# Performance work log

Hardware: AMD Instinct MI355X
Metric: run time of the kernel (lower is better)

The kernel has to match this reference:

```python
import jax, jax.numpy as jnp
import numpy as np
from jax import lax

B, C_IN, HC, H, W, K = 32, 32, 64, 64, 64, 3


def _conv(x, w, b):
    # x: [B,C,H,W], w: [O,I,K,K] -> [B,O,H,W] (stride 1, pad 1)
    y = lax.conv_general_dilated(x, w, window_strides=(1, 1), padding=[(1, 1), (1, 1)],
                                 dimension_numbers=("NCHW", "OIHW", "NCHW"))
    return y + b[None, :, None, None]


def setup_inputs() -> dict:
    key = jax.random.key(0)
    ks = jax.random.split(key, 20)
    d = {
        "x": jax.random.normal(ks[0], (B, C_IN, H, W), jnp.float32),
        "hidden_state": jax.random.normal(ks[1], (B, HC, H, W), jnp.float32),
        "cell_state": jax.random.normal(ks[2], (B, HC, H, W), jnp.float32),
    }
    sx = 1.0 / np.sqrt(C_IN * K * K)
    sh = 1.0 / np.sqrt(HC * K * K)
    names_x = ["w_xi", "w_xf", "w_xo", "w_xg"]
    names_h = ["w_hi", "w_hf", "w_ho", "w_hg"]
    for i, n in enumerate(names_x):
        d[n] = jax.random.uniform(ks[3 + i], (HC, C_IN, K, K), jnp.float32, -sx, sx)
        d["b" + n[1:]] = jax.random.uniform(ks[7 + i], (HC,), jnp.float32, -sx, sx)
    for i, n in enumerate(names_h):
        d[n] = jax.random.uniform(ks[11 + i], (HC, HC, K, K), jnp.float32, -sh, sh)
        d["b" + n[1:]] = jax.random.uniform(ks[15 + i], (HC,), jnp.float32, -sh, sh)
    return d


def reference(x, hidden_state, cell_state,
              w_xi, w_xf, w_xo, w_xg, b_xi, b_xf, b_xo, b_xg,
              w_hi, w_hf, w_ho, w_hg, b_hi, b_hf, b_ho, b_hg):
    Wx = jnp.concatenate([w_xi, w_xf, w_xo, w_xg], axis=0)
    bx = jnp.concatenate([b_xi, b_xf, b_xo, b_xg], axis=0)
    Wh = jnp.concatenate([w_hi, w_hf, w_ho, w_hg], axis=0)
    bh = jnp.concatenate([b_hi, b_hf, b_ho, b_hg], axis=0)
    gates = _conv(x, Wx, bx) + _conv(hidden_state, Wh, bh)  # [B,4*HC,H,W]
    zi, zf, zo, zg = jnp.split(gates, 4, axis=1)
    i = jax.nn.sigmoid(zi)
    f = jax.nn.sigmoid(zf)
    o = jax.nn.sigmoid(zo)
    g = jnp.tanh(zg)
    c_new = f * cell_state + i * g
    h_new = o * jnp.tanh(c_new)
    return (h_new, c_new)
```

## Files before the change

### kernel.cpp

```cpp
#include <hip/hip_runtime.h>


#define B_   32
#define CIN  32
#define HC_  64
#define HH   64
#define WW   64

#define A_ELEMS (9 * 6 * 8 * 64 * 8)
#define P_ROW   (12 * 66 * 8)
#define AKK     4096
#define BLDS    25344

typedef __attribute__((ext_vector_type(8)))  short  short8;
typedef __attribute__((ext_vector_type(16))) float  floatx16;

struct PackArgs {
    const float* wx[4]; const float* wh[4];
    const float* bx[4]; const float* bh[4];
};

__device__ __forceinline__ short f2bf(float f) {
    unsigned u = __float_as_uint(f);
    u += 0x7FFFu + ((u >> 16) & 1u);
    return (short)(u >> 16);
}

__device__ __forceinline__ void gl_lds16(const short* g, short* l) {
    __builtin_amdgcn_global_load_lds(
        (const __attribute__((address_space(1))) unsigned int*)g,
        (__attribute__((address_space(3))) unsigned int*)l, 16, 0, 0);
}

__global__ __launch_bounds__(256) void pack_weights(PackArgs pa, short* a_pk, float* bias) {
    int idx = blockIdx.x * 256 + threadIdx.x;
    if (idx < A_ELEMS) {
        int j    = idx & 7;
        int lane = (idx >> 3) & 63;
        int rest = idx >> 9;
        int s    = rest & 7;
        int rest2 = rest >> 3;
        int kk   = rest2 % 6;
        int tap  = rest2 / 6;
        int og = s >> 1, fi = s & 1;
        int m32 = lane & 31;
        int gate = 2 * fi + (m32 >> 4);
        int oc   = og * 16 + (m32 & 15);
        int c    = kk * 16 + (lane >> 5) * 8 + j;
        int ky = tap / 3, kx = tap - 3 * ky;
        float v = (c < CIN)
            ? pa.wx[gate][((oc * CIN + c) * 3 + ky) * 3 + kx]
            : pa.wh[gate][((oc * HC_ + (c - CIN)) * 3 + ky) * 3 + kx];
        a_pk[idx] = f2bf(v);
    }
    if (idx < 256) {
        int gate = idx >> 6, oc = idx & 63;
        bias[idx] = pa.bx[gate][oc] + pa.bh[gate][oc];
    }
}

__global__ __launch_bounds__(256) void pack_input(const float* __restrict__ x,
                                                  const float* __restrict__ h,
                                                  short* __restrict__ P) {
    const int yy = blockIdx.x, b = blockIdx.y;
    int4* prow4 = (int4*)(P + ((size_t)b * 66 + yy) * P_ROW);

    if (yy == 0 || yy == 65) {
        int4 z = {0, 0, 0, 0};
        for (int g = threadIdx.x; g < 792; g += 256) prow4[g] = z;
        return;
    }

    __shared__ short t[64 * 98];
    const int y = yy - 1;
    const int col = threadIdx.x & 63, cg = threadIdx.x >> 6;
    for (int c = cg; c < 96; c += 4) {
        float v = (c < CIN) ? x[((b * CIN + c) * HH + y) * WW + col]
                            : h[((b * HC_ + (c - CIN)) * HH + y) * WW + col];
        t[col * 98 + c] = f2bf(v);
    }
    __syncthreads();

    for (int g = threadIdx.x; g < 792; g += 256) {
        int pc = g / 66, xx = g - 66 * pc;
        int4 val = {0, 0, 0, 0};
        if (xx >= 1 && xx <= 64) {
            const short* sp = &t[(xx - 1) * 98 + pc * 8];
            val.x = *(const int*)(sp + 0); val.y = *(const int*)(sp + 2);
            val.z = *(const int*)(sp + 4); val.w = *(const int*)(sp + 6);
        }
        prow4[g] = val;
    }
}

__global__ __launch_bounds__(512, 4) void convlstm_main(
    const short* __restrict__ P, const short* __restrict__ a_pk,
    const float* __restrict__ bias, const float* __restrict__ cell,
    float* __restrict__ out)
{
    __shared__ __align__(16) short lds[BLDS + 3 * AKK];

    const int tid = threadIdx.x;
    const int b  = blockIdx.x >> 5;
    const int y0 = (blockIdx.x & 31) * 2;

    const int wv = tid >> 6, lane = tid & 63;
    const int ln31 = lane & 31, hg = lane >> 5;
    const int og = wv & 3, nh = wv >> 2;
    const int y = y0 + nh;

    floatx16 acc[2][2];
    #pragma unroll
    for (int fi = 0; fi < 2; ++fi)
        #pragma unroll
        for (int ns = 0; ns < 2; ++ns)
            #pragma unroll
            for (int q = 0; q < 16; ++q) acc[fi][ns][q] = 0.f;

    short* Asl = lds + BLDS;
    const int a_rd  = og * 1024 + lane * 8;
    const int b_rd  = nh * 6336 + hg * 528 + ln31 * 8;

    {
        const short* Bsrc = P + ((size_t)(b * 66) + y0) * P_ROW;
        #pragma unroll
        for (int i = 0; i < 7; ++i) {
            int id = i * 512 + tid;
            if (id < 3168)
                gl_lds16(Bsrc + id * 8, lds + (i * 512 + wv * 64) * 8);
        }
        gl_lds16(a_pk + tid * 8,       Asl + wv * 64 * 8);
        gl_lds16(a_pk + AKK + tid * 8, Asl + AKK + wv * 64 * 8);
    }
    asm volatile("s_waitcnt vmcnt(1)" ::: "memory");
    __builtin_amdgcn_s_barrier();
    __builtin_amdgcn_sched_barrier(0);

    #pragma unroll
    for (int c = 0; c < 54; ++c) {
        const int tap = c / 6, kk = c % 6;
        const int ky = tap / 3, kx = tap % 3;

        if (c < 52)
            gl_lds16(a_pk + (c + 2) * AKK + tid * 8,
                     Asl + ((c + 2) % 3) * AKK + wv * 64 * 8);

        const short* Ab = Asl + (c % 3) * AKK;
        const short* Bb = lds + b_rd + ky * 6336 + kk * 1056 + kx * 8;

        short8 a0 = *(const short8*)&Ab[a_rd];
        short8 a1 = *(const short8*)&Ab[a_rd + 512];
        short8 b0 = *(const short8*)&Bb[0];
        short8 b1 = *(const short8*)&Bb[256];
        acc[0][0] = __builtin_amdgcn_mfma_f32_32x32x16_bf16(a0, b0, acc[0][0], 0, 0, 0);
        acc[0][1] = __builtin_amdgcn_mfma_f32_32x32x16_bf16(a0, b1, acc[0][1], 0, 0, 0);
        acc[1][0] = __builtin_amdgcn_mfma_f32_32x32x16_bf16(a1, b0, acc[1][0], 0, 0, 0);
        acc[1][1] = __builtin_amdgcn_mfma_f32_32x32x16_bf16(a1, b1, acc[1][1], 0, 0, 0);

        if (c < 52)       asm volatile("s_waitcnt vmcnt(1)" ::: "memory");
        else if (c == 52) asm volatile("s_waitcnt vmcnt(0)" ::: "memory");
        if (c < 53) {
            __builtin_amdgcn_s_barrier();
            __builtin_amdgcn_sched_barrier(0);
        }
    }

    const size_t plane = (size_t)B_ * HC_ * HH * WW;
    #pragma unroll
    for (int q = 0; q < 4; ++q)
    #pragma unroll
    for (int b8 = 0; b8 < 2; ++b8) {
        const int oc16 = q + 4 * hg + 8 * b8;
        const int oc = og * 16 + oc16;
        const float Bi = bias[oc],       Bf = bias[64 + oc];
        const float Bo = bias[128 + oc], Bg = bias[192 + oc];
        const int r_lo = q + 4 * b8, r_hi = q + 4 * (2 + b8);
        #pragma unroll
        for (int ns = 0; ns < 2; ++ns) {
            float zi = acc[0][ns][r_lo] + Bi;
            float zf = acc[0][ns][r_hi] + Bf;
            float zo = acc[1][ns][r_lo] + Bo;
            float zg = acc[1][ns][r_hi] + Bg;
            float ig = 1.f / (1.f + __expf(-zi));
            float fg = 1.f / (1.f + __expf(-zf));
            float sg = 1.f / (1.f + __expf(-zo));
            float e2 = __expf(2.f * zg);
            float gg = 1.f - 2.f / (e2 + 1.f);
            const int x = ns * 32 + ln31;
            size_t off = ((size_t)(b * HC_ + oc) * HH + y) * WW + x;
            float cn = fg * cell[off] + ig * gg;
            float ec = __expf(2.f * cn);
            out[off] = sg * (1.f - 2.f / (ec + 1.f));
            out[plane + off] = cn;
        }
    }
}

extern "C" void kernel_launch(void* const* d_in, const int* in_sizes, int n_in,
                              void* d_out, int out_size, void* d_ws, size_t ws_size,
                              hipStream_t stream) {
    PackArgs pa;
    pa.wx[0] = (const float*)d_in[3];  pa.bx[0] = (const float*)d_in[4];
    pa.wx[1] = (const float*)d_in[5];  pa.bx[1] = (const float*)d_in[6];
    pa.wx[2] = (const float*)d_in[7];  pa.bx[2] = (const float*)d_in[8];
    pa.wx[3] = (const float*)d_in[9];  pa.bx[3] = (const float*)d_in[10];
    pa.wh[0] = (const float*)d_in[11]; pa.bh[0] = (const float*)d_in[12];
    pa.wh[1] = (const float*)d_in[13]; pa.bh[1] = (const float*)d_in[14];
    pa.wh[2] = (const float*)d_in[15]; pa.bh[2] = (const float*)d_in[16];
    pa.wh[3] = (const float*)d_in[17]; pa.bh[3] = (const float*)d_in[18];

    short* a_pk = (short*)d_ws;
    float* bias = (float*)((char*)d_ws + A_ELEMS * sizeof(short));
    short* P    = (short*)((char*)d_ws + 443392);

    pack_weights<<<dim3(A_ELEMS / 256), dim3(256), 0, stream>>>(pa, a_pk, bias);
    pack_input <<<dim3(66, B_), dim3(256), 0, stream>>>(
        (const float*)d_in[0], (const float*)d_in[1], P);
    convlstm_main<<<dim3(B_ * 32), dim3(512), 0, stream>>>(
        P, a_pk, bias, (const float*)d_in[2], (float*)d_out);
}
```

Baseline: 222.6 us.

## Shrink main kernel to four waves each computing two output rows

New measurement: 223.4 us. About the same (+0.4%).

```diff
diff --git a/kernel.cpp b/kernel.cpp
--- a/kernel.cpp
+++ b/kernel.cpp
@@ -93,7 +93,7 @@
     }
 }
 
-__global__ __launch_bounds__(512, 4) void convlstm_main(
+__global__ __launch_bounds__(256, 2) void convlstm_main(
     const short* __restrict__ P, const short* __restrict__ a_pk,
     const float* __restrict__ bias, const float* __restrict__ cell,
     float* __restrict__ out)
@@ -106,33 +106,38 @@
 
     const int wv = tid >> 6, lane = tid & 63;
     const int ln31 = lane & 31, hg = lane >> 5;
-    const int og = wv & 3, nh = wv >> 2;
-    const int y = y0 + nh;
-
-    floatx16 acc[2][2];
+    const int og = wv;
+
+    floatx16 acc[2][2][2];
     #pragma unroll
     for (int fi = 0; fi < 2; ++fi)
         #pragma unroll
-        for (int ns = 0; ns < 2; ++ns)
+        for (int rr = 0; rr < 2; ++rr)
             #pragma unroll
-            for (int q = 0; q < 16; ++q) acc[fi][ns][q] = 0.f;
+            for (int ns = 0; ns < 2; ++ns)
+                #pragma unroll
+                for (int q = 0; q < 16; ++q) acc[fi][rr][ns][q] = 0.f;
 
     short* Asl = lds + BLDS;
-    const int a_rd  = og * 1024 + lane * 8;
-    const int b_rd  = nh * 6336 + hg * 528 + ln31 * 8;
+    const int a_rd   = og * 1024 + lane * 8;
+    const int b_lane = hg * 528 + ln31 * 8;
 
     {
         const short* Bsrc = P + ((size_t)(b * 66) + y0) * P_ROW;
         #pragma unroll
-        for (int i = 0; i < 7; ++i) {
-            int id = i * 512 + tid;
+        for (int i = 0; i < 13; ++i) {
+            int id = i * 256 + tid;
             if (id < 3168)
-                gl_lds16(Bsrc + id * 8, lds + (i * 512 + wv * 64) * 8);
-        }
-        gl_lds16(a_pk + tid * 8,       Asl + wv * 64 * 8);
-        gl_lds16(a_pk + AKK + tid * 8, Asl + AKK + wv * 64 * 8);
-    }
-    asm volatile("s_waitcnt vmcnt(1)" ::: "memory");
+                gl_lds16(Bsrc + id * 8, lds + (i * 256 + wv * 64) * 8);
+        }
+        #pragma unroll
+        for (int ck = 0; ck < 2; ++ck)
+            #pragma unroll
+            for (int i = 0; i < 2; ++i)
+                gl_lds16(a_pk + ck * AKK + (i * 256 + tid) * 8,
+                         Asl + ck * AKK + (i * 256 + wv * 64) * 8);
+    }
+    asm volatile("s_waitcnt vmcnt(2)" ::: "memory");
     __builtin_amdgcn_s_barrier();
     __builtin_amdgcn_sched_barrier(0);
 
@@ -141,23 +146,35 @@
         const int tap = c / 6, kk = c % 6;
         const int ky = tap / 3, kx = tap % 3;
 
-        if (c < 52)
-            gl_lds16(a_pk + (c + 2) * AKK + tid * 8,
-                     Asl + ((c + 2) % 3) * AKK + wv * 64 * 8);
-
-        const short* Ab = Asl + (c % 3) * AKK;
-        const short* Bb = lds + b_rd + ky * 6336 + kk * 1056 + kx * 8;
-
-        short8 a0 = *(const short8*)&Ab[a_rd];
-        short8 a1 = *(const short8*)&Ab[a_rd + 512];
-        short8 b0 = *(const short8*)&Bb[0];
-        short8 b1 = *(const short8*)&Bb[256];
-        acc[0][0] = __builtin_amdgcn_mfma_f32_32x32x16_bf16(a0, b0, acc[0][0], 0, 0, 0);
-        acc[0][1] = __builtin_amdgcn_mfma_f32_32x32x16_bf16(a0, b1, acc[0][1], 0, 0, 0);
-        acc[1][0] = __builtin_amdgcn_mfma_f32_32x32x16_bf16(a1, b0, acc[1][0], 0, 0, 0);
-        acc[1][1] = __builtin_amdgcn_mfma_f32_32x32x16_bf16(a1, b1, acc[1][1], 0, 0, 0);
-
-        if (c < 52)       asm volatile("s_waitcnt vmcnt(1)" ::: "memory");
+        if (c < 52) {
+            const short* src = a_pk + (c + 2) * AKK;
+            short* dst = Asl + ((c + 2) % 3) * AKK;
+            gl_lds16(src + tid * 8,         dst + (wv * 64) * 8);
+            gl_lds16(src + (256 + tid) * 8, dst + (256 + wv * 64) * 8);
+        }
+
+        const short* Ab = Asl + (c % 3) * AKK + a_rd;
+        const short* Bb = lds + b_lane + ky * 6336 + 2 * kk * 528 + kx * 8;
+
+        short8 a0  = *(const short8*)&Ab[0];
+        short8 a1  = *(const short8*)&Ab[512];
+        short8 b00 = *(const short8*)&Bb[0];
+        short8 b01 = *(const short8*)&Bb[256];
+        short8 b10 = *(const short8*)&Bb[6336];
+        short8 b11 = *(const short8*)&Bb[6336 + 256];
+
+        __builtin_amdgcn_s_setprio(1);
+        acc[0][0][0] = __builtin_amdgcn_mfma_f32_32x32x16_bf16(a0, b00, acc[0][0][0], 0, 0, 0);
+        acc[0][0][1] = __builtin_amdgcn_mfma_f32_32x32x16_bf16(a0, b01, acc[0][0][1], 0, 0, 0);
+        acc[0][1][0] = __builtin_amdgcn_mfma_f32_32x32x16_bf16(a0, b10, acc[0][1][0], 0, 0, 0);
+        acc[0][1][1] = __builtin_amdgcn_mfma_f32_32x32x16_bf16(a0, b11, acc[0][1][1], 0, 0, 0);
+        acc[1][0][0] = __builtin_amdgcn_mfma_f32_32x32x16_bf16(a1, b00, acc[1][0][0], 0, 0, 0);
+        acc[1][0][1] = __builtin_amdgcn_mfma_f32_32x32x16_bf16(a1, b01, acc[1][0][1], 0, 0, 0);
+        acc[1][1][0] = __builtin_amdgcn_mfma_f32_32x32x16_bf16(a1, b10, acc[1][1][0], 0, 0, 0);
+        acc[1][1][1] = __builtin_amdgcn_mfma_f32_32x32x16_bf16(a1, b11, acc[1][1][1], 0, 0, 0);
+        __builtin_amdgcn_s_setprio(0);
+
+        if (c < 52)       asm volatile("s_waitcnt vmcnt(2)" ::: "memory");
         else if (c == 52) asm volatile("s_waitcnt vmcnt(0)" ::: "memory");
         if (c < 53) {
             __builtin_amdgcn_s_barrier();
@@ -176,17 +193,20 @@
         const float Bo = bias[128 + oc], Bg = bias[192 + oc];
         const int r_lo = q + 4 * b8, r_hi = q + 4 * (2 + b8);
         #pragma unroll
+        for (int rr = 0; rr < 2; ++rr)
+        #pragma unroll
         for (int ns = 0; ns < 2; ++ns) {
-            float zi = acc[0][ns][r_lo] + Bi;
-            float zf = acc[0][ns][r_hi] + Bf;
-            float zo = acc[1][ns][r_lo] + Bo;
-            float zg = acc[1][ns][r_hi] + Bg;
+            float zi = acc[0][rr][ns][r_lo] + Bi;
+            float zf = acc[0][rr][ns][r_hi] + Bf;
+            float zo = acc[1][rr][ns][r_lo] + Bo;
+            float zg = acc[1][rr][ns][r_hi] + Bg;
             float ig = 1.f / (1.f + __expf(-zi));
             float fg = 1.f / (1.f + __expf(-zf));
             float sg = 1.f / (1.f + __expf(-zo));
             float e2 = __expf(2.f * zg);
             float gg = 1.f - 2.f / (e2 + 1.f);
             const int x = ns * 32 + ln31;
+            const int y = y0 + rr;
             size_t off = ((size_t)(b * HC_ + oc) * HH + y) * WW + x;
             float cn = fg * cell[off] + ig * gg;
             float ec = __expf(2.f * cn);
@@ -216,6 +236,6 @@
     pack_weights<<<dim3(A_ELEMS / 256), dim3(256), 0, stream>>>(pa, a_pk, bias);
     pack_input <<<dim3(66, B_), dim3(256), 0, stream>>>(
         (const float*)d_in[0], (const float*)d_in[1], P);
-    convlstm_main<<<dim3(B_ * 32), dim3(512), 0, stream>>>(
+    convlstm_main<<<dim3(B_ * 32), dim3(256), 0, stream>>>(
         P, a_pk, bias, (const float*)d_in[2], (float*)d_out);
 }
```

## Read weight fragments directly from global memory instead of LDS ring buffer

Applied to the files above, without the earlier changes.

Result: slower. 245.8 us (+10.4%).

```diff
diff --git a/kernel.cpp b/kernel.cpp
--- a/kernel.cpp
+++ b/kernel.cpp
@@ -98,7 +98,7 @@
     const float* __restrict__ bias, const float* __restrict__ cell,
     float* __restrict__ out)
 {
-    __shared__ __align__(16) short lds[BLDS + 3 * AKK];
+    __shared__ __align__(16) short lds[BLDS];
 
     const int tid = threadIdx.x;
     const int b  = blockIdx.x >> 5;
@@ -117,9 +117,8 @@
             #pragma unroll
             for (int q = 0; q < 16; ++q) acc[fi][ns][q] = 0.f;
 
-    short* Asl = lds + BLDS;
-    const int a_rd  = og * 1024 + lane * 8;
-    const int b_rd  = nh * 6336 + hg * 528 + ln31 * 8;
+    const short* Ag  = a_pk + og * 1024 + lane * 8;
+    const int    b_rd = nh * 6336 + hg * 528 + ln31 * 8;
 
     {
         const short* Bsrc = P + ((size_t)(b * 66) + y0) * P_ROW;
@@ -129,39 +128,24 @@
             if (id < 3168)
                 gl_lds16(Bsrc + id * 8, lds + (i * 512 + wv * 64) * 8);
         }
-        gl_lds16(a_pk + tid * 8,       Asl + wv * 64 * 8);
-        gl_lds16(a_pk + AKK + tid * 8, Asl + AKK + wv * 64 * 8);
-    }
-    asm volatile("s_waitcnt vmcnt(1)" ::: "memory");
-    __builtin_amdgcn_s_barrier();
-    __builtin_amdgcn_sched_barrier(0);
-
-    #pragma unroll
-    for (int c = 0; c < 54; ++c) {
-        const int tap = c / 6, kk = c % 6;
+    }
+    __syncthreads();
+
+    for (int tap = 0; tap < 9; ++tap) {
         const int ky = tap / 3, kx = tap % 3;
-
-        if (c < 52)
-            gl_lds16(a_pk + (c + 2) * AKK + tid * 8,
-                     Asl + ((c + 2) % 3) * AKK + wv * 64 * 8);
-
-        const short* Ab = Asl + (c % 3) * AKK;
-        const short* Bb = lds + b_rd + ky * 6336 + kk * 1056 + kx * 8;
-
-        short8 a0 = *(const short8*)&Ab[a_rd];
-        short8 a1 = *(const short8*)&Ab[a_rd + 512];
-        short8 b0 = *(const short8*)&Bb[0];
-        short8 b1 = *(const short8*)&Bb[256];
-        acc[0][0] = __builtin_amdgcn_mfma_f32_32x32x16_bf16(a0, b0, acc[0][0], 0, 0, 0);
-        acc[0][1] = __builtin_amdgcn_mfma_f32_32x32x16_bf16(a0, b1, acc[0][1], 0, 0, 0);
-        acc[1][0] = __builtin_amdgcn_mfma_f32_32x32x16_bf16(a1, b0, acc[1][0], 0, 0, 0);
-        acc[1][1] = __builtin_amdgcn_mfma_f32_32x32x16_bf16(a1, b1, acc[1][1], 0, 0, 0);
-
-        if (c < 52)       asm volatile("s_waitcnt vmcnt(1)" ::: "memory");
-        else if (c == 52) asm volatile("s_waitcnt vmcnt(0)" ::: "memory");
-        if (c < 53) {
-            __builtin_amdgcn_s_barrier();
-            __builtin_amdgcn_sched_barrier(0);
+        const short* Bb = lds + b_rd + ky * 6336 + kx * 8;
+        const short* Ac = Ag + tap * 6 * AKK;
+
+        #pragma unroll
+        for (int kk = 0; kk < 6; ++kk) {
+            short8 a0 = *(const short8*)&Ac[kk * AKK];
+            short8 a1 = *(const short8*)&Ac[kk * AKK + 512];
+            short8 b0 = *(const short8*)&Bb[kk * 1056];
+            short8 b1 = *(const short8*)&Bb[kk * 1056 + 256];
+            acc[0][0] = __builtin_amdgcn_mfma_f32_32x32x16_bf16(a0, b0, acc[0][0], 0, 0, 0);
+            acc[0][1] = __builtin_amdgcn_mfma_f32_32x32x16_bf16(a0, b1, acc[0][1], 0, 0, 0);
+            acc[1][0] = __builtin_amdgcn_mfma_f32_32x32x16_bf16(a1, b0, acc[1][0], 0, 0, 0);
+            acc[1][1] = __builtin_amdgcn_mfma_f32_32x32x16_bf16(a1, b1, acc[1][1], 0, 0, 0);
         }
     }
 
```
